# Performance work log

Measured on AMD Instinct MI355X. Metric: run time of the kernel, lower is better.

Reference implementation:

```python
import jax, jax.numpy as jnp
import numpy as np

B, S, D = 4, 2048, 1024

def setup_inputs() -> dict:
    key = jax.random.key(0)
    k0, k1, k2, k3 = jax.random.split(key, 4)
    scale = 1.0 / np.sqrt(D)
    return {
        "x": jax.random.normal(k0, (B, S, D), dtype=jnp.float32),
        "Wq": jax.random.normal(k1, (D, D), dtype=jnp.float32) * scale,
        "Wk": jax.random.normal(k2, (D, D), dtype=jnp.float32) * scale,
        "Wv": jax.random.normal(k3, (D, D), dtype=jnp.float32) * scale,
    }

def reference(x, Wq, Wk, Wv):
    # x: [B,S,D]; Wq/Wk/Wv: [D_in, D_out] (equivalent to torch Linear weight transposed)
    q = jnp.einsum('bsd,de->bse', x, Wq)
    k = jnp.einsum('bsd,de->bse', x, Wk)
    v = jnp.einsum('bsd,de->bse', x, Wv)
    d_out = k.shape[-1]
    scores = jnp.einsum('bqe,bke->bqk', q, k)  # [B,S,S]
    S_ = scores.shape[-1]
    causal = jnp.tril(jnp.ones((S_, S_), dtype=bool))  # True = keep
    # masked_fill before scaling == after scaling (-inf invariant under positive scale)
    scores = jnp.where(causal, scores, -jnp.inf)
    attn = jax.nn.softmax(scores / jnp.sqrt(jnp.asarray(d_out, scores.dtype)), axis=-1)
    # dropout p=0.0 -> identity
    return jnp.einsum('bqk,bke->bqe', attn, v)
```

## Files before the change

kernel.cpp:

```cpp
#include <hip/hip_runtime.h>

#define B_  4
#define S_  2048
#define D_  1024
#define N_  (B_*S_)
#define SCALE 0.03125f
#define NEGINF (-3.0e38f)

typedef unsigned short u16;
typedef __attribute__((ext_vector_type(8))) short short8;
typedef __attribute__((ext_vector_type(4))) float floatx4;

__device__ __forceinline__ u16 f2bf(float f) {
    unsigned int u = __float_as_uint(f);
    u += 0x7FFFu + ((u >> 16) & 1u);
    return (u16)(u >> 16);
}
__device__ __forceinline__ float bf2f(u16 h) {
    return __uint_as_float((unsigned int)h << 16);
}

__device__ __forceinline__ void gl_lds16(const void* g, void* l) {
    __builtin_amdgcn_global_load_lds(
        (const __attribute__((address_space(1))) unsigned int*)g,
        (__attribute__((address_space(3))) unsigned int*)l, 16, 0, 0);
}

__device__ __forceinline__ int xcd_chunk(int bid, int nwg) {
    return (bid & 7) * (nwg >> 3) + (bid >> 3);
}

__global__ __launch_bounds__(256) void cast_fused(const float* __restrict__ x,
                                                  const float* __restrict__ Wq, const float* __restrict__ Wk,
                                                  const float* __restrict__ Wv,
                                                  u16* __restrict__ xb, u16* __restrict__ Wqb,
                                                  u16* __restrict__ Wkb, u16* __restrict__ Wvt) {
    __shared__ float t[32][33];
    const int blk = blockIdx.x;
    if (blk < 5120) {
        const float* src; u16* dst; size_t i;
        if (blk < 4096)      { src = x;  dst = xb;  i = (size_t)blk * 2048; }
        else if (blk < 4608) { src = Wq; dst = Wqb; i = (size_t)(blk - 4096) * 2048; }
        else                 { src = Wk; dst = Wkb; i = (size_t)(blk - 4608) * 2048; }
        i += (size_t)threadIdx.x * 8;
        float4 a = *(const float4*)&src[i];
        float4 b = *(const float4*)&src[i + 4];
        short8 o;
        o[0]=f2bf(a.x); o[1]=f2bf(a.y); o[2]=f2bf(a.z); o[3]=f2bf(a.w);
        o[4]=f2bf(b.x); o[5]=f2bf(b.y); o[6]=f2bf(b.z); o[7]=f2bf(b.w);
        *(short8*)&dst[i] = o;
    } else {
        const int tb = blk - 5120;
        const int c = threadIdx.x & 31, r0 = threadIdx.x >> 5;
        const int i0 = (tb >> 5) * 32, j0 = (tb & 31) * 32;
#pragma unroll
        for (int rr = 0; rr < 4; ++rr)
            t[r0 + rr * 8][c] = Wv[(size_t)(i0 + r0 + rr * 8) * D_ + j0 + c];
        __syncthreads();
#pragma unroll
        for (int rr = 0; rr < 4; ++rr)
            Wvt[(size_t)(j0 + r0 + rr * 8) * D_ + i0 + c] = f2bf(t[c][r0 + rr * 8]);
    }
}


__device__ __forceinline__ void mfma_nt_128(const u16* __restrict__ A, int lda,
                                            const u16* __restrict__ Bp, int ldb,
                                            int m0, int n0, int kext,
                                            u16* Sh, floatx4 acc[4][4])
{
    const int tid  = threadIdx.x;
    const int lane = tid & 63;
    const int lr   = lane & 15, quad = lane >> 4;
    const int wm   = ((tid >> 6) & 1) * 64, wn = (tid >> 7) * 64;
    const int nt   = kext >> 6;

    auto stage1 = [&](int t, int h) {
        const int kk = h >> 2, mat = (h >> 1) & 1, half = h & 1;
        const int idx = tid * 8;
        const int row = half * 64 + (idx >> 5);
        const int s   = (idx & 31) >> 3;
        const int gk  = (t << 6) + kk * 32 + ((s ^ ((row >> 1) & 3)) << 3);
        u16* dst = Sh + (t & 1) * 16384 + mat * 8192 + kk * 4096 + half * 2048 + idx;
        const u16* src = mat ? &Bp[(size_t)(n0 + row) * ldb + gk]
                             : &A [(size_t)(m0 + row) * lda + gk];
        gl_lds16(src, dst);
    };

#pragma unroll
    for (int h = 0; h < 8; ++h) stage1(0, h);

    for (int t = 0; t < nt; ++t) {
        const u16* buf = Sh + (t & 1) * 16384;
        const bool pf = (t + 1 < nt);
#pragma unroll
        for (int p = 0; p < 2; ++p) {
            if (pf) {
#pragma unroll
                for (int h = 0; h < 4; ++h) stage1(t + 1, p * 4 + h);
                asm volatile("s_waitcnt vmcnt(8)" ::: "memory");
            } else if (p == 0) {
                asm volatile("s_waitcnt vmcnt(4)" ::: "memory");
            } else {
                asm volatile("s_waitcnt vmcnt(0)" ::: "memory");
            }
            __builtin_amdgcn_s_barrier();

            short8 af[4], bf[4];
#pragma unroll
            for (int i = 0; i < 4; ++i) {
                const int ar = wm + i * 16 + lr;
                af[i] = *(const short8*)&buf[p * 4096 + ar * 32 + ((quad ^ ((ar >> 1) & 3)) << 3)];
                const int br = wn + i * 16 + lr;
                bf[i] = *(const short8*)&buf[8192 + p * 4096 + br * 32 + ((quad ^ ((br >> 1) & 3)) << 3)];
            }
            asm volatile("s_waitcnt lgkmcnt(0)" ::: "memory");
            __builtin_amdgcn_s_setprio(1);
#pragma unroll
            for (int i = 0; i < 4; ++i)
#pragma unroll
                for (int j = 0; j < 4; ++j)
                    acc[i][j] = __builtin_amdgcn_mfma_f32_16x16x32_bf16(af[i], bf[j], acc[i][j], 0, 0, 0);
            __builtin_amdgcn_s_setprio(0);
            __builtin_amdgcn_s_barrier();
        }
    }
}

#define EPI_VARS                                              \
    const int lane = threadIdx.x & 63;                        \
    const int lr = lane & 15, quad = lane >> 4;               \
    const int wm = ((threadIdx.x >> 6) & 1) * 64, wn = (threadIdx.x >> 7) * 64;

__device__ __forceinline__ void mfma_nt_128w8(const u16* __restrict__ A, int lda,
                                              const u16* __restrict__ Bp, int ldb,
                                              int m0, int n0, int kext,
                                              u16* Sh, floatx4 acc[2][4])
{
    const int tid  = threadIdx.x;
    const int lane = tid & 63;
    const int lr   = lane & 15, quad = lane >> 4;
    const int wid  = tid >> 6;
    const int wm   = (wid >> 1) * 32;
    const int wn   = (wid & 1) * 64;
    const int nt   = kext >> 6;

    auto stage1 = [&](int t, int h) {
        const int kk = h >> 1, mat = h & 1;
        const int idx = tid * 8;
        const int row = idx >> 5;
        const int s   = (idx & 31) >> 3;
        const int gk  = (t << 6) + kk * 32 + ((s ^ ((row >> 1) & 3)) << 3);
        u16* dst = Sh + (t & 1) * 16384 + mat * 8192 + kk * 4096 + idx;
        const u16* src = mat ? &Bp[(size_t)(n0 + row) * ldb + gk]
                             : &A [(size_t)(m0 + row) * lda + gk];
        gl_lds16(src, dst);
    };

#pragma unroll
    for (int h = 0; h < 4; ++h) stage1(0, h);

    for (int t = 0; t < nt; ++t) {
        const u16* buf = Sh + (t & 1) * 16384;
        const bool pf = (t + 1 < nt);
#pragma unroll
        for (int p = 0; p < 2; ++p) {
            if (pf) {
                stage1(t + 1, p * 2); stage1(t + 1, p * 2 + 1);
                asm volatile("s_waitcnt vmcnt(4)" ::: "memory");
            } else if (p == 0) {
                asm volatile("s_waitcnt vmcnt(2)" ::: "memory");
            } else {
                asm volatile("s_waitcnt vmcnt(0)" ::: "memory");
            }
            __builtin_amdgcn_s_barrier();

            short8 af[2], bf[4];
#pragma unroll
            for (int i = 0; i < 2; ++i) {
                const int ar = wm + i * 16 + lr;
                af[i] = *(const short8*)&buf[p * 4096 + ar * 32 + ((quad ^ ((ar >> 1) & 3)) << 3)];
            }
#pragma unroll
            for (int j = 0; j < 4; ++j) {
                const int br = wn + j * 16 + lr;
                bf[j] = *(const short8*)&buf[8192 + p * 4096 + br * 32 + ((quad ^ ((br >> 1) & 3)) << 3)];
            }
            asm volatile("s_waitcnt lgkmcnt(0)" ::: "memory");
            __builtin_amdgcn_s_setprio(1);
#pragma unroll
            for (int i = 0; i < 2; ++i)
#pragma unroll
                for (int j = 0; j < 4; ++j)
                    acc[i][j] = __builtin_amdgcn_mfma_f32_16x16x32_bf16(af[i], bf[j], acc[i][j], 0, 0, 0);
            __builtin_amdgcn_s_setprio(0);
            __builtin_amdgcn_s_barrier();
        }
    }
}

__device__ __forceinline__ void mfma_nt_256(const u16* __restrict__ A, int lda,
                                            const u16* __restrict__ Bp, int ldb,
                                            int m0, int n0, int kext,
                                            u16* Sh, floatx4 acc[8][4])
{
    const int tid  = threadIdx.x;
    const int lane = tid & 63;
    const int lr   = lane & 15, quad = lane >> 4;
    const int wr   = (tid >> 8) & 1, wc = (tid >> 6) & 3;
    const int nt   = kext >> 6;

    auto stage1 = [&](int t, int h) {
        const int kk = h >> 2, mat = (h >> 1) & 1, half = h & 1;
        const int idx = tid * 8;
        const int row = half * 128 + (idx >> 5);
        const int s   = (idx & 31) >> 3;
        const int gk  = (t << 6) + kk * 32 + ((s ^ ((row >> 1) & 3)) << 3);
        u16* dst = Sh + (t & 1) * 32768 + mat * 16384 + kk * 8192 + half * 4096 + idx;
        const u16* src = mat ? &Bp[(size_t)(n0 + row) * ldb + gk]
                             : &A [(size_t)(m0 + row) * lda + gk];
        gl_lds16(src, dst);
    };

#pragma unroll
    for (int h = 0; h < 8; ++h) stage1(0, h);

    for (int t = 0; t < nt; ++t) {
        const u16* buf = Sh + (t & 1) * 32768;
        const bool pf = (t + 1 < nt);
        short8 af[4], bf[4];

        if (pf) { stage1(t + 1, 0); stage1(t + 1, 1);
                  asm volatile("s_waitcnt vmcnt(6)" ::: "memory"); }
        else      asm volatile("s_waitcnt vmcnt(4)" ::: "memory");
        __builtin_amdgcn_s_barrier();
#pragma unroll
        for (int i = 0; i < 4; ++i) {
            const int ar = wr * 128 + i * 16 + lr;
            af[i] = *(const short8*)&buf[ar * 32 + ((quad ^ ((ar >> 1) & 3)) << 3)];
            const int br = wc * 64 + i * 16 + lr;
            bf[i] = *(const short8*)&buf[16384 + br * 32 + ((quad ^ ((br >> 1) & 3)) << 3)];
        }
        asm volatile("s_waitcnt lgkmcnt(0)" ::: "memory");
        __builtin_amdgcn_s_setprio(1);
#pragma unroll
        for (int i = 0; i < 4; ++i)
#pragma unroll
            for (int j = 0; j < 4; ++j)
                acc[i][j] = __builtin_amdgcn_mfma_f32_16x16x32_bf16(af[i], bf[j], acc[i][j], 0, 0, 0);
        __builtin_amdgcn_s_setprio(0);
        __builtin_amdgcn_s_barrier();

#pragma unroll
        for (int i = 0; i < 4; ++i) {
            const int ar = wr * 128 + 64 + i * 16 + lr;
            af[i] = *(const short8*)&buf[ar * 32 + ((quad ^ ((ar >> 1) & 3)) << 3)];
        }
        if (pf) { stage1(t + 1, 2); stage1(t + 1, 3); }
        __builtin_amdgcn_s_barrier();
        asm volatile("s_waitcnt lgkmcnt(0)" ::: "memory");
        __builtin_amdgcn_s_setprio(1);
#pragma unroll
        for (int i = 0; i < 4; ++i)
#pragma unroll
            for (int j = 0; j < 4; ++j)
                acc[4 + i][j] = __builtin_amdgcn_mfma_f32_16x16x32_bf16(af[i], bf[j], acc[4 + i][j], 0, 0, 0);
        __builtin_amdgcn_s_setprio(0);
        __builtin_amdgcn_s_barrier();

        if (pf) { stage1(t + 1, 4); stage1(t + 1, 5);
                  asm volatile("s_waitcnt vmcnt(6)" ::: "memory"); }
        else      asm volatile("s_waitcnt vmcnt(0)" ::: "memory");
        __builtin_amdgcn_s_barrier();
#pragma unroll
        for (int i = 0; i < 4; ++i) {
            const int ar = wr * 128 + i * 16 + lr;
            af[i] = *(const short8*)&buf[8192 + ar * 32 + ((quad ^ ((ar >> 1) & 3)) << 3)];
            const int br = wc * 64 + i * 16 + lr;
            bf[i] = *(const short8*)&buf[24576 + br * 32 + ((quad ^ ((br >> 1) & 3)) << 3)];
        }
        asm volatile("s_waitcnt lgkmcnt(0)" ::: "memory");
        __builtin_amdgcn_s_setprio(1);
#pragma unroll
        for (int i = 0; i < 4; ++i)
#pragma unroll
            for (int j = 0; j < 4; ++j)
                acc[i][j] = __builtin_amdgcn_mfma_f32_16x16x32_bf16(af[i], bf[j], acc[i][j], 0, 0, 0);
        __builtin_amdgcn_s_setprio(0);
        __builtin_amdgcn_s_barrier();

#pragma unroll
        for (int i = 0; i < 4; ++i) {
            const int ar = wr * 128 + 64 + i * 16 + lr;
            af[i] = *(const short8*)&buf[8192 + ar * 32 + ((quad ^ ((ar >> 1) & 3)) << 3)];
        }
        if (pf) { stage1(t + 1, 6); stage1(t + 1, 7); }
        __builtin_amdgcn_s_barrier();
        asm volatile("s_waitcnt lgkmcnt(0)" ::: "memory");
        __builtin_amdgcn_s_setprio(1);
#pragma unroll
        for (int i = 0; i < 4; ++i)
#pragma unroll
            for (int j = 0; j < 4; ++j)
                acc[4 + i][j] = __builtin_amdgcn_mfma_f32_16x16x32_bf16(af[i], bf[j], acc[4 + i][j], 0, 0, 0);
        __builtin_amdgcn_s_setprio(0);
        __builtin_amdgcn_s_barrier();
    }
}

#define EPI256_VARS                                           \
    const int lane = threadIdx.x & 63;                        \
    const int lr = lane & 15, quad = lane >> 4;               \
    const int wr = (threadIdx.x >> 8) & 1, wc = (threadIdx.x >> 6) & 3;

__global__ __launch_bounds__(256) void mt_mfma(const u16* __restrict__ Wkb, const u16* __restrict__ Wqb,
                                               u16* __restrict__ Mt)
{
    __shared__ u16 Sh[32768];
    const int m0 = blockIdx.y * 128, n0 = blockIdx.x * 128;
    floatx4 acc[4][4];
#pragma unroll
    for (int i = 0; i < 4; ++i)
#pragma unroll
        for (int j = 0; j < 4; ++j) acc[i][j] = (floatx4){0.f, 0.f, 0.f, 0.f};
    mfma_nt_128(Wkb, D_, Wqb, D_, m0, n0, D_, Sh, acc);

    EPI_VARS
#pragma unroll
    for (int i = 0; i < 4; ++i)
#pragma unroll
        for (int j = 0; j < 4; ++j)
#pragma unroll
            for (int r = 0; r < 4; ++r)
                Mt[(size_t)(m0 + wm + i * 16 + quad * 4 + r) * D_ + n0 + wn + j * 16 + lr] = f2bf(acc[i][j][r]);
}

__global__ __launch_bounds__(512, 2) void yv_mfma(const u16* __restrict__ xb, const u16* __restrict__ Mt,
                                                  const u16* __restrict__ Wvt,
                                                  u16* __restrict__ Y, u16* __restrict__ Vt)
{
    __shared__ u16 Sh[65536];
    const int lid = xcd_chunk(blockIdx.x, 256);
    floatx4 acc[8][4];
#pragma unroll
    for (int i = 0; i < 8; ++i)
#pragma unroll
        for (int j = 0; j < 4; ++j) acc[i][j] = (floatx4){0.f, 0.f, 0.f, 0.f};

    if (lid < 128) {
        const int m0 = (lid >> 2) * 256, n0 = (lid & 3) * 256;
        mfma_nt_256(xb, D_, Mt, D_, m0, n0, D_, Sh, acc);
        EPI256_VARS
#pragma unroll
        for (int i = 0; i < 8; ++i)
#pragma unroll
            for (int j = 0; j < 4; ++j)
#pragma unroll
                for (int r = 0; r < 4; ++r)
                    Y[(size_t)(m0 + wr * 128 + i * 16 + quad * 4 + r) * D_ + n0 + wc * 64 + j * 16 + lr]
                        = f2bf(acc[i][j][r]);
    } else {
        const int v = lid - 128;
        const int b = v >> 5;
        const int mloc = ((v >> 2) & 7) * 256;
        const int n0 = (v & 3) * 256;
        const int m0 = b * S_ + mloc;
        u16* Vb = Vt + (size_t)b * D_ * S_;
        mfma_nt_256(xb, D_, Wvt, D_, m0, n0, D_, Sh, acc);
        EPI256_VARS
#pragma unroll
        for (int i = 0; i < 8; ++i)
#pragma unroll
            for (int j = 0; j < 4; ++j) {
                const int ee = n0 + wc * 64 + j * 16 + lr;
                const int s4 = mloc + wr * 128 + i * 16 + quad * 4;
                ushort4 o;
                o.x = f2bf(acc[i][j][0]); o.y = f2bf(acc[i][j][1]);
                o.z = f2bf(acc[i][j][2]); o.w = f2bf(acc[i][j][3]);
                *(ushort4*)&Vb[(size_t)ee * S_ + s4] = o;
            }
    }
}

__global__ __launch_bounds__(512, 2) void scores_mfma(const u16* __restrict__ Y, const u16* __restrict__ xb,
                                                      u16* __restrict__ Sc)
{
    __shared__ u16 Sh[65536];
    const int lid = xcd_chunk(blockIdx.x, 144);
    const int b = lid / 36;
    const int t = lid - b * 36;
    int qt = 0;
    while ((qt + 1) * (qt + 2) / 2 <= t) ++qt;
    const int kt = t - qt * (qt + 1) / 2;

    const u16* A  = Y  + (size_t)b * S_ * D_;
    const u16* Bp = xb + (size_t)b * S_ * D_;
    u16* Sb = Sc + (size_t)b * S_ * S_;
    const int m0 = qt * 256, n0 = kt * 256;
    floatx4 acc[8][4];
#pragma unroll
    for (int i = 0; i < 8; ++i)
#pragma unroll
        for (int j = 0; j < 4; ++j) acc[i][j] = (floatx4){0.f, 0.f, 0.f, 0.f};
    mfma_nt_256(A, D_, Bp, D_, m0, n0, D_, Sh, acc);

    EPI256_VARS
#pragma unroll
    for (int i = 0; i < 8; ++i)
#pragma unroll
        for (int r = 0; r < 4; ++r) {
            const int grow = m0 + wr * 128 + i * 16 + quad * 4 + r;
#pragma unroll
            for (int j = 0; j < 4; ++j) {
                const int gcol = n0 + wc * 64 + j * 16 + lr;
                const float v = (gcol <= grow) ? acc[i][j][r] * SCALE : NEGINF;
                Sb[(size_t)grow * S_ + gcol] = f2bf(v);
            }
        }
}

__global__ __launch_bounds__(256) void softmax_k(const u16* __restrict__ Sc, u16* __restrict__ P)
{
    const int row = blockIdx.x * 4 + (threadIdx.x >> 6);
    const int lane = threadIdx.x & 63;
    const int b = row >> 11, q = row & (S_ - 1);
    const int L = ((q >> 7) + 1) << 7;
    const u16* rp = Sc + ((size_t)b * S_ + q) * S_;
    u16* pp = P + ((size_t)b * S_ + q) * S_;

    float f[4][8];
    float lmax = -3.4e38f;
#pragma unroll
    for (int c = 0; c < 4; ++c) {
        const int i = c * 512 + lane * 8;
        if (i < L) {
            short8 v = *(const short8*)&rp[i];
#pragma unroll
            for (int k = 0; k < 8; ++k) { f[c][k] = bf2f((u16)v[k]); lmax = fmaxf(lmax, f[c][k]); }
        }
    }
#pragma unroll
    for (int off = 32; off; off >>= 1) lmax = fmaxf(lmax, __shfl_xor(lmax, off, 64));

    float lsum = 0.f;
#pragma unroll
    for (int c = 0; c < 4; ++c) {
        const int i = c * 512 + lane * 8;
        if (i < L) {
#pragma unroll
            for (int k = 0; k < 8; ++k) { f[c][k] = __expf(f[c][k] - lmax); lsum += f[c][k]; }
        }
    }
#pragma unroll
    for (int off = 32; off; off >>= 1) lsum += __shfl_xor(lsum, off, 64);
    const float inv = 1.0f / lsum;

#pragma unroll
    for (int c = 0; c < 4; ++c) {
        const int i = c * 512 + lane * 8;
        if (i < L) {
            short8 o;
#pragma unroll
            for (int k = 0; k < 8; ++k) o[k] = (short)f2bf(f[c][k] * inv);
            *(short8*)&pp[i] = o;
        }
    }
}

__device__ __forceinline__ void pv_epi(floatx4 acc[2][4], int b, int m0, int n0, float* __restrict__ O)
{
    const int lane = threadIdx.x & 63;
    const int lr = lane & 15, quad = lane >> 4;
    const int wid = threadIdx.x >> 6;
    const int wm = (wid >> 1) * 32, wn = (wid & 1) * 64;
#pragma unroll
    for (int i = 0; i < 2; ++i)
#pragma unroll
        for (int r = 0; r < 4; ++r) {
            const int grow = m0 + wm + i * 16 + quad * 4 + r;
#pragma unroll
            for (int j = 0; j < 4; ++j)
                O[((size_t)b * S_ + grow) * D_ + n0 + wn + j * 16 + lr] = acc[i][j][r];
        }
}

__global__ __launch_bounds__(512, 2) void pv_mfma(const u16* __restrict__ P, const u16* __restrict__ Vt,
                                                  float* __restrict__ O)
{
    __shared__ u16 Sh[32768];
    const int lid = xcd_chunk(blockIdx.x, 256);
    const int b  = lid >> 6;
    const int et = (lid >> 3) & 7;
    const int pr = lid & 7;
    const int n0 = et * 128;
    const u16* A  = P  + (size_t)b * S_ * S_;
    const u16* Bp = Vt + (size_t)b * D_ * S_;

    floatx4 acc[2][4];
    const int qtA = pr, qtB = 15 - pr;

#pragma unroll
    for (int i = 0; i < 2; ++i)
#pragma unroll
        for (int j = 0; j < 4; ++j) acc[i][j] = (floatx4){0.f, 0.f, 0.f, 0.f};
    mfma_nt_128w8(A, S_, Bp, S_, qtA * 128, n0, (qtA + 1) * 128, Sh, acc);
    pv_epi(acc, b, qtA * 128, n0, O);

#pragma unroll
    for (int i = 0; i < 2; ++i)
#pragma unroll
        for (int j = 0; j < 4; ++j) acc[i][j] = (floatx4){0.f, 0.f, 0.f, 0.f};
    mfma_nt_128w8(A, S_, Bp, S_, qtB * 128, n0, (qtB + 1) * 128, Sh, acc);
    pv_epi(acc, b, qtB * 128, n0, O);
}

extern "C" void kernel_launch(void* const* d_in, const int* in_sizes, int n_in,
                              void* d_out, int out_size, void* d_ws, size_t ws_size,
                              hipStream_t stream) {
    const float* x  = (const float*)d_in[0];
    const float* Wq = (const float*)d_in[1];
    const float* Wk = (const float*)d_in[2];
    const float* Wv = (const float*)d_in[3];
    float* out = (float*)d_out;
    char* w = (char*)d_ws;

    u16* xb  = (u16*)(w);
    u16* Wqb = (u16*)(w + 16777216);
    u16* Wkb = (u16*)(w + 18874368);
    u16* Wvt = (u16*)(w + 20971520);
    u16* Mt  = (u16*)(w + 23068672);
    u16* Y   = (u16*)(w + 25165824);
    u16* Vt  = (u16*)(w + 41943040);
    u16* Sc  = (u16*)(w + 58720256);
    u16* P   = (u16*)(w + 92274688);

    cast_fused <<<dim3(6144),   256, 0, stream>>>(x, Wq, Wk, Wv, xb, Wqb, Wkb, Wvt);
    mt_mfma    <<<dim3(8, 8),   256, 0, stream>>>(Wkb, Wqb, Mt);
    yv_mfma    <<<dim3(256),    512, 0, stream>>>(xb, Mt, Wvt, Y, Vt);
    scores_mfma<<<dim3(144),    512, 0, stream>>>(Y, xb, Sc);
    softmax_k  <<<dim3(N_/4),   256, 0, stream>>>(Sc, P);
    pv_mfma    <<<dim3(256),    512, 0, stream>>>(P, Vt, out);
}
```

Before: 208.4 us.

## Simplify GEMM K-loop pipelining to one barrier per tile with whole-tile prefetch

Rewrites the three MFMA GEMM mainloops so each K tile begins with a full vmcnt(0) wait and a single barrier, then issues the whole next-tile prefetch at once and runs both k-halves without intermediate barriers or explicit lgkmcnt waits. The aim is to cut barrier count and let the compiler schedule LDS reads and MFMAs freely. In exchange, the fine-grained interleaving of partial prefetches with compute is lost, and waiting on all outstanding loads each tile may expose more global-load latency.

```diff
diff --git a/kernel.cpp b/kernel.cpp
--- a/kernel.cpp
+++ b/kernel.cpp
@@ -75,46 +75,37 @@
     const int wm   = ((tid >> 6) & 1) * 64, wn = (tid >> 7) * 64;
     const int nt   = kext >> 6;
 
-    auto stage1 = [&](int t, int h) {
-        const int kk = h >> 2, mat = (h >> 1) & 1, half = h & 1;
-        const int idx = tid * 8;
-        const int row = half * 64 + (idx >> 5);
-        const int s   = (idx & 31) >> 3;
-        const int gk  = (t << 6) + kk * 32 + ((s ^ ((row >> 1) & 3)) << 3);
-        u16* dst = Sh + (t & 1) * 16384 + mat * 8192 + kk * 4096 + half * 2048 + idx;
-        const u16* src = mat ? &Bp[(size_t)(n0 + row) * ldb + gk]
-                             : &A [(size_t)(m0 + row) * lda + gk];
-        gl_lds16(src, dst);
+    auto stage8 = [&](int t) {
+#pragma unroll
+        for (int h = 0; h < 8; ++h) {
+            const int kk = h >> 2, mat = (h >> 1) & 1, half = h & 1;
+            const int idx = tid * 8;
+            const int row = half * 64 + (idx >> 5);
+            const int s   = (idx & 31) >> 3;
+            const int gk  = (t << 6) + kk * 32 + ((s ^ ((row >> 1) & 3)) << 3);
+            u16* dst = Sh + (t & 1) * 16384 + mat * 8192 + kk * 4096 + half * 2048 + idx;
+            const u16* src = mat ? &Bp[(size_t)(n0 + row) * ldb + gk]
+                                 : &A [(size_t)(m0 + row) * lda + gk];
+            gl_lds16(src, dst);
+        }
     };
 
-#pragma unroll
-    for (int h = 0; h < 8; ++h) stage1(0, h);
-
+    stage8(0);
     for (int t = 0; t < nt; ++t) {
+        asm volatile("s_waitcnt vmcnt(0)" ::: "memory");
+        __builtin_amdgcn_s_barrier();
+        if (t + 1 < nt) stage8(t + 1);
         const u16* buf = Sh + (t & 1) * 16384;
-        const bool pf = (t + 1 < nt);
-#pragma unroll
-        for (int p = 0; p < 2; ++p) {
-            if (pf) {
-#pragma unroll
-                for (int h = 0; h < 4; ++h) stage1(t + 1, p * 4 + h);
-                asm volatile("s_waitcnt vmcnt(8)" ::: "memory");
-            } else if (p == 0) {
-                asm volatile("s_waitcnt vmcnt(4)" ::: "memory");
-            } else {
-                asm volatile("s_waitcnt vmcnt(0)" ::: "memory");
-            }
-            __builtin_amdgcn_s_barrier();
-
+#pragma unroll
+        for (int kk = 0; kk < 2; ++kk) {
             short8 af[4], bf[4];
 #pragma unroll
             for (int i = 0; i < 4; ++i) {
                 const int ar = wm + i * 16 + lr;
-                af[i] = *(const short8*)&buf[p * 4096 + ar * 32 + ((quad ^ ((ar >> 1) & 3)) << 3)];
+                af[i] = *(const short8*)&buf[kk * 4096 + ar * 32 + ((quad ^ ((ar >> 1) & 3)) << 3)];
                 const int br = wn + i * 16 + lr;
-                bf[i] = *(const short8*)&buf[8192 + p * 4096 + br * 32 + ((quad ^ ((br >> 1) & 3)) << 3)];
-            }
-            asm volatile("s_waitcnt lgkmcnt(0)" ::: "memory");
+                bf[i] = *(const short8*)&buf[8192 + kk * 4096 + br * 32 + ((quad ^ ((br >> 1) & 3)) << 3)];
+            }
             __builtin_amdgcn_s_setprio(1);
 #pragma unroll
             for (int i = 0; i < 4; ++i)
@@ -122,7 +113,6 @@
                 for (int j = 0; j < 4; ++j)
                     acc[i][j] = __builtin_amdgcn_mfma_f32_16x16x32_bf16(af[i], bf[j], acc[i][j], 0, 0, 0);
             __builtin_amdgcn_s_setprio(0);
-            __builtin_amdgcn_s_barrier();
         }
     }
 }
@@ -145,48 +135,40 @@
     const int wn   = (wid & 1) * 64;
     const int nt   = kext >> 6;
 
-    auto stage1 = [&](int t, int h) {
-        const int kk = h >> 1, mat = h & 1;
-        const int idx = tid * 8;
-        const int row = idx >> 5;
-        const int s   = (idx & 31) >> 3;
-        const int gk  = (t << 6) + kk * 32 + ((s ^ ((row >> 1) & 3)) << 3);
-        u16* dst = Sh + (t & 1) * 16384 + mat * 8192 + kk * 4096 + idx;
-        const u16* src = mat ? &Bp[(size_t)(n0 + row) * ldb + gk]
-                             : &A [(size_t)(m0 + row) * lda + gk];
-        gl_lds16(src, dst);
+    auto stage4 = [&](int t) {
+#pragma unroll
+        for (int h = 0; h < 4; ++h) {
+            const int kk = h >> 1, mat = h & 1;
+            const int idx = tid * 8;
+            const int row = idx >> 5;
+            const int s   = (idx & 31) >> 3;
+            const int gk  = (t << 6) + kk * 32 + ((s ^ ((row >> 1) & 3)) << 3);
+            u16* dst = Sh + (t & 1) * 16384 + mat * 8192 + kk * 4096 + idx;
+            const u16* src = mat ? &Bp[(size_t)(n0 + row) * ldb + gk]
+                                 : &A [(size_t)(m0 + row) * lda + gk];
+            gl_lds16(src, dst);
+        }
     };
 
-#pragma unroll
-    for (int h = 0; h < 4; ++h) stage1(0, h);
-
+    stage4(0);
     for (int t = 0; t < nt; ++t) {
+        asm volatile("s_waitcnt vmcnt(0)" ::: "memory");
+        __builtin_amdgcn_s_barrier();
+        if (t + 1 < nt) stage4(t + 1);
         const u16* buf = Sh + (t & 1) * 16384;
-        const bool pf = (t + 1 < nt);
-#pragma unroll
-        for (int p = 0; p < 2; ++p) {
-            if (pf) {
-                stage1(t + 1, p * 2); stage1(t + 1, p * 2 + 1);
-                asm volatile("s_waitcnt vmcnt(4)" ::: "memory");
-            } else if (p == 0) {
-                asm volatile("s_waitcnt vmcnt(2)" ::: "memory");
-            } else {
-                asm volatile("s_waitcnt vmcnt(0)" ::: "memory");
-            }
-            __builtin_amdgcn_s_barrier();
-
+#pragma unroll
+        for (int kk = 0; kk < 2; ++kk) {
             short8 af[2], bf[4];
 #pragma unroll
             for (int i = 0; i < 2; ++i) {
                 const int ar = wm + i * 16 + lr;
-                af[i] = *(const short8*)&buf[p * 4096 + ar * 32 + ((quad ^ ((ar >> 1) & 3)) << 3)];
+                af[i] = *(const short8*)&buf[kk * 4096 + ar * 32 + ((quad ^ ((ar >> 1) & 3)) << 3)];
             }
 #pragma unroll
             for (int j = 0; j < 4; ++j) {
                 const int br = wn + j * 16 + lr;
-                bf[j] = *(const short8*)&buf[8192 + p * 4096 + br * 32 + ((quad ^ ((br >> 1) & 3)) << 3)];
-            }
-            asm volatile("s_waitcnt lgkmcnt(0)" ::: "memory");
+                bf[j] = *(const short8*)&buf[8192 + kk * 4096 + br * 32 + ((quad ^ ((br >> 1) & 3)) << 3)];
+            }
             __builtin_amdgcn_s_setprio(1);
 #pragma unroll
             for (int i = 0; i < 2; ++i)
@@ -194,7 +176,6 @@
                 for (int j = 0; j < 4; ++j)
                     acc[i][j] = __builtin_amdgcn_mfma_f32_16x16x32_bf16(af[i], bf[j], acc[i][j], 0, 0, 0);
             __builtin_amdgcn_s_setprio(0);
-            __builtin_amdgcn_s_barrier();
         }
     }
 }
@@ -210,101 +191,48 @@
     const int wr   = (tid >> 8) & 1, wc = (tid >> 6) & 3;
     const int nt   = kext >> 6;
 
-    auto stage1 = [&](int t, int h) {
-        const int kk = h >> 2, mat = (h >> 1) & 1, half = h & 1;
-        const int idx = tid * 8;
-        const int row = half * 128 + (idx >> 5);
-        const int s   = (idx & 31) >> 3;
-        const int gk  = (t << 6) + kk * 32 + ((s ^ ((row >> 1) & 3)) << 3);
-        u16* dst = Sh + (t & 1) * 32768 + mat * 16384 + kk * 8192 + half * 4096 + idx;
-        const u16* src = mat ? &Bp[(size_t)(n0 + row) * ldb + gk]
-                             : &A [(size_t)(m0 + row) * lda + gk];
-        gl_lds16(src, dst);
+    auto stage8 = [&](int t) {
+#pragma unroll
+        for (int h = 0; h < 8; ++h) {
+            const int kk = h >> 2, mat = (h >> 1) & 1, half = h & 1;
+            const int idx = tid * 8;
+            const int row = half * 128 + (idx >> 5);
+            const int s   = (idx & 31) >> 3;
+            const int gk  = (t << 6) + kk * 32 + ((s ^ ((row >> 1) & 3)) << 3);
+            u16* dst = Sh + (t & 1) * 32768 + mat * 16384 + kk * 8192 + half * 4096 + idx;
+            const u16* src = mat ? &Bp[(size_t)(n0 + row) * ldb + gk]
+                                 : &A [(size_t)(m0 + row) * lda + gk];
+            gl_lds16(src, dst);
+        }
     };
 
-#pragma unroll
-    for (int h = 0; h < 8; ++h) stage1(0, h);
-
+    stage8(0);
     for (int t = 0; t < nt; ++t) {
+        asm volatile("s_waitcnt vmcnt(0)" ::: "memory");
+        __builtin_amdgcn_s_barrier();
+        if (t + 1 < nt) stage8(t + 1);
         const u16* buf = Sh + (t & 1) * 32768;
-        const bool pf = (t + 1 < nt);
-        short8 af[4], bf[4];
-
-        if (pf) { stage1(t + 1, 0); stage1(t + 1, 1);
-                  asm volatile("s_waitcnt vmcnt(6)" ::: "memory"); }
-        else      asm volatile("s_waitcnt vmcnt(4)" ::: "memory");
-        __builtin_amdgcn_s_barrier();
-#pragma unroll
-        for (int i = 0; i < 4; ++i) {
-            const int ar = wr * 128 + i * 16 + lr;
-            af[i] = *(const short8*)&buf[ar * 32 + ((quad ^ ((ar >> 1) & 3)) << 3)];
-            const int br = wc * 64 + i * 16 + lr;
-            bf[i] = *(const short8*)&buf[16384 + br * 32 + ((quad ^ ((br >> 1) & 3)) << 3)];
-        }
-        asm volatile("s_waitcnt lgkmcnt(0)" ::: "memory");
-        __builtin_amdgcn_s_setprio(1);
-#pragma unroll
-        for (int i = 0; i < 4; ++i)
-#pragma unroll
-            for (int j = 0; j < 4; ++j)
-                acc[i][j] = __builtin_amdgcn_mfma_f32_16x16x32_bf16(af[i], bf[j], acc[i][j], 0, 0, 0);
-        __builtin_amdgcn_s_setprio(0);
-        __builtin_amdgcn_s_barrier();
-
-#pragma unroll
-        for (int i = 0; i < 4; ++i) {
-            const int ar = wr * 128 + 64 + i * 16 + lr;
-            af[i] = *(const short8*)&buf[ar * 32 + ((quad ^ ((ar >> 1) & 3)) << 3)];
-        }
-        if (pf) { stage1(t + 1, 2); stage1(t + 1, 3); }
-        __builtin_amdgcn_s_barrier();
-        asm volatile("s_waitcnt lgkmcnt(0)" ::: "memory");
-        __builtin_amdgcn_s_setprio(1);
-#pragma unroll
-        for (int i = 0; i < 4; ++i)
-#pragma unroll
-            for (int j = 0; j < 4; ++j)
-                acc[4 + i][j] = __builtin_amdgcn_mfma_f32_16x16x32_bf16(af[i], bf[j], acc[4 + i][j], 0, 0, 0);
-        __builtin_amdgcn_s_setprio(0);
-        __builtin_amdgcn_s_barrier();
-
-        if (pf) { stage1(t + 1, 4); stage1(t + 1, 5);
-                  asm volatile("s_waitcnt vmcnt(6)" ::: "memory"); }
-        else      asm volatile("s_waitcnt vmcnt(0)" ::: "memory");
-        __builtin_amdgcn_s_barrier();
-#pragma unroll
-        for (int i = 0; i < 4; ++i) {
-            const int ar = wr * 128 + i * 16 + lr;
-            af[i] = *(const short8*)&buf[8192 + ar * 32 + ((quad ^ ((ar >> 1) & 3)) << 3)];
-            const int br = wc * 64 + i * 16 + lr;
-            bf[i] = *(const short8*)&buf[24576 + br * 32 + ((quad ^ ((br >> 1) & 3)) << 3)];
-        }
-        asm volatile("s_waitcnt lgkmcnt(0)" ::: "memory");
-        __builtin_amdgcn_s_setprio(1);
-#pragma unroll
-        for (int i = 0; i < 4; ++i)
-#pragma unroll
-            for (int j = 0; j < 4; ++j)
-                acc[i][j] = __builtin_amdgcn_mfma_f32_16x16x32_bf16(af[i], bf[j], acc[i][j], 0, 0, 0);
-        __builtin_amdgcn_s_setprio(0);
-        __builtin_amdgcn_s_barrier();
-
-#pragma unroll
-        for (int i = 0; i < 4; ++i) {
-            const int ar = wr * 128 + 64 + i * 16 + lr;
-            af[i] = *(const short8*)&buf[8192 + ar * 32 + ((quad ^ ((ar >> 1) & 3)) << 3)];
-        }
-        if (pf) { stage1(t + 1, 6); stage1(t + 1, 7); }
-        __builtin_amdgcn_s_barrier();
-        asm volatile("s_waitcnt lgkmcnt(0)" ::: "memory");
-        __builtin_amdgcn_s_setprio(1);
-#pragma unroll
-        for (int i = 0; i < 4; ++i)
-#pragma unroll
-            for (int j = 0; j < 4; ++j)
-                acc[4 + i][j] = __builtin_amdgcn_mfma_f32_16x16x32_bf16(af[i], bf[j], acc[4 + i][j], 0, 0, 0);
-        __builtin_amdgcn_s_setprio(0);
-        __builtin_amdgcn_s_barrier();
+#pragma unroll
+        for (int kk = 0; kk < 2; ++kk) {
+            short8 af[8], bf[4];
+#pragma unroll
+            for (int i = 0; i < 8; ++i) {
+                const int ar = wr * 128 + i * 16 + lr;
+                af[i] = *(const short8*)&buf[kk * 8192 + ar * 32 + ((quad ^ ((ar >> 1) & 3)) << 3)];
+            }
+#pragma unroll
+            for (int j = 0; j < 4; ++j) {
+                const int br = wc * 64 + j * 16 + lr;
+                bf[j] = *(const short8*)&buf[16384 + kk * 8192 + br * 32 + ((quad ^ ((br >> 1) & 3)) << 3)];
+            }
+            __builtin_amdgcn_s_setprio(1);
+#pragma unroll
+            for (int i = 0; i < 8; ++i)
+#pragma unroll
+                for (int j = 0; j < 4; ++j)
+                    acc[i][j] = __builtin_amdgcn_mfma_f32_16x16x32_bf16(af[i], bf[j], acc[i][j], 0, 0, 0);
+            __builtin_amdgcn_s_setprio(0);
+        }
     }
 }
 
```

After: 211.0 us. Within noise of the previous version (+1.2%).
